# Kernel tuning notes

Measured on AMD Instinct MI355X. Metric: run time of the kernel, lower is better.

Reference implementation:

```python
import jax, jax.numpy as jnp
import numpy as np
from jax import lax

DN = ('NCHW', 'OIHW', 'NCHW')
EPS = 1e-5


def _conv3x3(x, w, b):
    return lax.conv_general_dilated(x, w, (1, 1), 'SAME', dimension_numbers=DN) + b[:, None, None]


def _conv1x1(x, w, b):
    return jnp.einsum('bchw,oc->bohw', x, w) + b[:, None, None]


def _dwconv3x3(x, w, b):
    # w: (C,1,3,3), depthwise
    C = x.shape[1]
    return lax.conv_general_dilated(x, w, (1, 1), 'SAME', feature_group_count=C,
                                    dimension_numbers=DN) + b[:, None, None]


def setup_inputs() -> dict:
    key = jax.random.key(0)
    ks = jax.random.split(key, 24)
    b, t, c, h, w = 2, 8, 64, 160, 160
    r, K = c // 4, 3

    def n(k, shape, s=0.05):
        return jax.random.normal(k, shape, dtype=jnp.float32) * s

    return {
        'feature': n(ks[0], (b, t, c, h, w), 1.0),
        'kc_w1': n(ks[1], (r, c)),
        'kc_bn_gamma': jnp.ones((r,), jnp.float32),
        'kc_bn_beta': jnp.zeros((r,), jnp.float32),
        'kc_bn_mean': jnp.zeros((r,), jnp.float32),
        'kc_bn_var': jnp.ones((r,), jnp.float32),
        'kc_w2': n(ks[2], (c * K * K, r)),
        'kc_b2': n(ks[3], (c * K * K,)),
        'kc_bias': n(ks[4], (c,)),
        'conv1_w': n(ks[5], (2 * c, 2 * c, 3, 3)),
        'conv1_b': n(ks[6], (2 * c,)),
        'pi1_w': n(ks[7], (4 * c, c)),
        'pi1_b': n(ks[8], (4 * c,)),
        'dw1_w': n(ks[9], (4 * c, 1, 3, 3)),
        'dw1_b': n(ks[10], (4 * c,)),
        'po1_w': n(ks[11], (c, 4 * c)),
        'po1_b': n(ks[12], (c,)),
        'pi2_w': n(ks[13], (4 * c, c)),
        'pi2_b': n(ks[14], (4 * c,)),
        'dw2_w': n(ks[15], (4 * c, 1, 3, 3)),
        'dw2_b': n(ks[16], (4 * c,)),
        'po2_w': n(ks[17], (c, 4 * c)),
        'po2_b': n(ks[18], (c,)),
    }


def reference(feature, kc_w1, kc_bn_gamma, kc_bn_beta, kc_bn_mean, kc_bn_var,
              kc_w2, kc_b2, kc_bias, conv1_w, conv1_b,
              pi1_w, pi1_b, dw1_w, dw1_b, po1_w, po1_b,
              pi2_w, pi2_b, dw2_w, dw2_b, po2_w, po2_b):
    b, t, c, h, w = feature.shape
    K = int(round((kc_w2.shape[0] // c) ** 0.5))  # dynamic kernel size (3)

    def dyn_dwconv(x_feat, y):
        # kernel generation: GAP -> 1x1 -> BN(eval) -> ReLU -> 1x1
        pool = x_feat.mean(axis=(2, 3))                           # (b, c)
        z = pool @ kc_w1.T                                        # (b, r)
        z = (z - kc_bn_mean) * jax.lax.rsqrt(kc_bn_var + EPS) * kc_bn_gamma + kc_bn_beta
        z = jax.nn.relu(z)
        wd = (z @ kc_w2.T + kc_b2).reshape(b, c, K, K)            # per-sample dw kernels

        def per_sample(yi, wi):
            return lax.conv_general_dilated(yi[None], wi[:, None], (1, 1), 'SAME',
                                            feature_group_count=c,
                                            dimension_numbers=DN)[0]
        out = jax.vmap(per_sample)(y, wd)                         # (b, c, h, w)
        return out + kc_bias[None, :, None, None]

    def step(feat_prop, x_feat):
        fp = dyn_dwconv(x_feat, feat_prop)
        fusion = jnp.concatenate([x_feat, fp], axis=1)
        fusion = jax.nn.leaky_relu(_conv3x3(fusion, conv1_w, conv1_b), 0.1)
        f1, f2 = fusion[:, :c], fusion[:, c:]
        g1 = jax.nn.sigmoid(_conv1x1(_dwconv3x3(_conv1x1(f1, pi1_w, pi1_b), dw1_w, dw1_b), po1_w, po1_b))
        g2 = jax.nn.sigmoid(_conv1x1(_dwconv3x3(_conv1x1(f2, pi2_w, pi2_b), dw2_w, dw2_b), po2_w, po2_b))
        new_fp = f1 * g1 + f2 * g2
        return new_fp, new_fp

    init = feature[:, t - 1]                                      # frame t-1
    xs = jnp.moveaxis(jnp.flip(feature[:, :t - 1], axis=1), 1, 0)  # frames t-2 .. 0
    _, ys = lax.scan(step, init, xs)                              # (t-1, b, c, h, w)
    full = jnp.concatenate([jnp.flip(ys, axis=0), init[None]], axis=0)
    return jnp.moveaxis(full, 0, 1)                               # (b, t, c, h, w)
```

## Files before the change

### kernel.cpp

```cpp
#include <hip/hip_runtime.h>

typedef __attribute__((ext_vector_type(8))) __bf16 bf16x8;
typedef __attribute__((ext_vector_type(4))) float f32x4;

#define BB 2
#define TT 8
#define CC 64
#define HH 160
#define WW 160
#define HWW 25600
#define RR 16
#define C2 128
#define C4 256
#define C8 512
#define NSTEP 7
#define CHW (CC*HWW)
#define EPSV 1e-5f

__device__ __forceinline__ f32x4 mfma16(bf16x8 a, bf16x8 b, f32x4 c) {
    return __builtin_amdgcn_mfma_f32_16x16x32_bf16(a, b, c, 0, 0, 0);
}

__global__ void pool_kernel(const float* __restrict__ feat, float* __restrict__ pool) {
    int idx = blockIdx.x;
    int b = idx / (NSTEP * CC);
    int f = (idx / CC) % NSTEP;
    int c = idx % CC;
    const float4* src = (const float4*)(feat + ((size_t)(b * TT + f) * CC + c) * HWW);
    float s = 0.f;
    for (int i = threadIdx.x; i < HWW / 4; i += 256) {
        float4 v = src[i];
        s += v.x + v.y + v.z + v.w;
    }
    __shared__ float sm[256];
    sm[threadIdx.x] = s;
    __syncthreads();
    for (int off = 128; off > 0; off >>= 1) {
        if (threadIdx.x < off) sm[threadIdx.x] += sm[threadIdx.x + off];
        __syncthreads();
    }
    if (threadIdx.x == 0) pool[idx] = sm[0] * (1.0f / HWW);
}

__global__ void wd_kernel(const float* __restrict__ pool, const float* __restrict__ w1,
                          const float* __restrict__ gamma, const float* __restrict__ beta,
                          const float* __restrict__ mean, const float* __restrict__ var,
                          const float* __restrict__ w2, const float* __restrict__ b2,
                          float* __restrict__ wdT) {
    int bf = blockIdx.x;
    __shared__ float z[RR];
    int tid = threadIdx.x;
    if (tid < RR) {
        const float* p = pool + bf * CC;
        float s = 0.f;
        for (int c = 0; c < CC; c++) s += p[c] * w1[tid * CC + c];
        s = (s - mean[tid]) * rsqrtf(var[tid] + EPSV) * gamma[tid] + beta[tid];
        z[tid] = s > 0.f ? s : 0.f;
    }
    __syncthreads();
    for (int o = tid; o < CC * 9; o += 64) {
        float s = b2[o];
        #pragma unroll
        for (int r = 0; r < RR; r++) s += z[r] * w2[o * RR + r];
        int c = o / 9, t = o % 9;
        wdT[bf * 576 + t * CC + c] = s;
    }
}

__global__ void copy_init_kernel(const float* __restrict__ feat, float* __restrict__ out) {
    int i = blockIdx.x * 256 + threadIdx.x;
    int n4 = CHW / 4;
    int b = i / n4;
    int r = i % n4;
    size_t off = ((size_t)(b * TT + (TT - 1)) * CHW) / 4 + r;
    ((float4*)out)[off] = ((const float4*)feat)[off];
}

__global__ void prep_weights(const float* __restrict__ c1w,
                             const float* __restrict__ pi1, const float* __restrict__ pi2,
                             const float* __restrict__ po1, const float* __restrict__ po2,
                             const float* __restrict__ dw1, const float* __restrict__ dw2,
                             const float* __restrict__ dw1b, const float* __restrict__ dw2b,
                             __bf16* __restrict__ Bc1,
                             __bf16* __restrict__ Bpi1, __bf16* __restrict__ Bpi2,
                             __bf16* __restrict__ Bpo1, __bf16* __restrict__ Bpo2,
                             float* __restrict__ dwT12, float* __restrict__ dwb12) {
    int idx = blockIdx.x * 256 + threadIdx.x;
    if (idx < 147456) {
        int oc = idx / 1152, k = idx % 1152;
        int t = k >> 7, ic = k & 127;
        Bc1[idx] = (__bf16)c1w[(oc * 128 + ic) * 9 + t];
        return;
    }
    idx -= 147456;
    if (idx < 16384) { Bpi1[idx] = (__bf16)pi1[idx]; return; }
    idx -= 16384;
    if (idx < 16384) { Bpi2[idx] = (__bf16)pi2[idx]; return; }
    idx -= 16384;
    if (idx < 16384) { Bpo1[idx] = (__bf16)po1[idx]; return; }
    idx -= 16384;
    if (idx < 16384) { Bpo2[idx] = (__bf16)po2[idx]; return; }
    idx -= 16384;
    if (idx < 4608) {
        int t = idx / 512, c = idx % 512;
        dwT12[t * C8 + c] = (c < 256) ? dw1[c * 9 + t] : dw2[(c - 256) * 9 + t];
        return;
    }
    idx -= 4608;
    if (idx < 512) { dwb12[idx] = (idx < 256) ? dw1b[idx] : dw2b[idx - 256]; }
}

__global__ void featPM_kernel(const float* __restrict__ feat, __bf16* __restrict__ featPM) {
    __shared__ float Lt[64 * 68];
    int bf = blockIdx.x / 400;
    int p0 = (blockIdx.x % 400) * 64;
    int tid = threadIdx.x;
    int c = tid & 63, half = tid >> 6;
    const float* src = feat + ((size_t)bf * CC + c) * HWW + p0 + half * 16;
    #pragma unroll
    for (int k = 0; k < 16; k++) Lt[(half * 16 + k) * 68 + c] = src[k];
    __syncthreads();
    int cg = tid & 7;
    #pragma unroll
    for (int pass = 0; pass < 2; pass++) {
        int pl = (tid >> 3) + pass * 32;
        bf16x8 o;
        #pragma unroll
        for (int j = 0; j < 8; j++) o[j] = (__bf16)Lt[pl * 68 + cg * 8 + j];
        *(bf16x8*)(featPM + ((size_t)bf * HWW + p0 + pl) * CC + cg * 8) = o;
    }
}

__global__ void dyndw_kernel(const __bf16* __restrict__ src, size_t bstr,
                             const float* __restrict__ wdT, const float* __restrict__ kc_bias,
                             __bf16* __restrict__ fpPM, int fx) {
    int gi = blockIdx.x * 256 + threadIdx.x;
    int c0 = (gi & 7) * 8;
    int rem = gi >> 3;
    int p = rem % HWW;
    int bb = rem / HWW;
    int py = p / WW, px = p % WW;
    float acc[8];
    float4 k0 = *(const float4*)(kc_bias + c0);
    float4 k1 = *(const float4*)(kc_bias + c0 + 4);
    acc[0]=k0.x; acc[1]=k0.y; acc[2]=k0.z; acc[3]=k0.w;
    acc[4]=k1.x; acc[5]=k1.y; acc[6]=k1.z; acc[7]=k1.w;
    const float* wb = wdT + (size_t)(bb * NSTEP + fx) * 576;
    const __bf16* sb = src + (size_t)bb * bstr;
    const int dyA[9] = {-1,-1,-1,0,0,0,1,1,1};
    const int dxA[9] = {-1,0,1,-1,0,1,-1,0,1};
    #pragma unroll
    for (int t = 0; t < 9; t++) {
        int dy = dyA[t], dx = dxA[t];
        if ((unsigned)(py + dy) < HH && (unsigned)(px + dx) < WW) {
            bf16x8 uv = *(const bf16x8*)(sb + (size_t)(p + dy * WW + dx) * CC + c0);
            float4 w0 = *(const float4*)(wb + t * CC + c0);
            float4 w1 = *(const float4*)(wb + t * CC + c0 + 4);
            acc[0] += (float)uv[0] * w0.x; acc[1] += (float)uv[1] * w0.y;
            acc[2] += (float)uv[2] * w0.z; acc[3] += (float)uv[3] * w0.w;
            acc[4] += (float)uv[4] * w1.x; acc[5] += (float)uv[5] * w1.y;
            acc[6] += (float)uv[6] * w1.z; acc[7] += (float)uv[7] * w1.w;
        }
    }
    bf16x8 o;
    #pragma unroll
    for (int j = 0; j < 8; j++) o[j] = (__bf16)acc[j];
    *(bf16x8*)(fpPM + ((size_t)bb * HWW + p) * CC + c0) = o;
}

__global__ void conv1_gemm(const __bf16* __restrict__ featPM, const __bf16* __restrict__ fpPM,
                           const __bf16* __restrict__ Bc1, const float* __restrict__ bias,
                           __bf16* __restrict__ fusionPM, int fx) {
    __shared__ __align__(16) __bf16 As[128 * 40];
    __shared__ __align__(16) __bf16 Bs[128 * 40];
    const int tid = threadIdx.x;
    const int bb = blockIdx.x / 200;
    const int p0 = (blockIdx.x % 200) * 128;
    const int i = tid >> 1, h = tid & 1;
    const int p = p0 + i;
    const int py = p / WW, px = p % WW;
    const __bf16* featB = featPM + (size_t)(bb * TT + fx) * HWW * CC;
    const __bf16* fpB   = fpPM + (size_t)bb * HWW * CC;
    const int wv = tid >> 6, lane = tid & 63, lm = lane & 15, lq = lane >> 4;
    f32x4 acc[2][8];
    #pragma unroll
    for (int mt = 0; mt < 2; mt++)
        #pragma unroll
        for (int nt = 0; nt < 8; nt++) acc[mt][nt] = (f32x4){0.f, 0.f, 0.f, 0.f};

    for (int ks = 0; ks < 36; ks++) {
        const int t = ks >> 2, ci0 = (ks & 3) * 32;
        const int dy = t / 3 - 1, dx = t % 3 - 1;
        const bool valid = ((unsigned)(py + dy) < HH) && ((unsigned)(px + dx) < WW);
        uint4 a0 = {0,0,0,0}, a1 = {0,0,0,0};
        if (valid) {
            const __bf16* sp = (ci0 < 64)
                ? featB + (size_t)(p + dy * WW + dx) * CC + ci0
                : fpB   + (size_t)(p + dy * WW + dx) * CC + (ci0 - 64);
            a0 = *(const uint4*)(sp + h * 16);
            a1 = *(const uint4*)(sp + h * 16 + 8);
        }
        const __bf16* bp = Bc1 + (size_t)i * 1152 + ks * 32 + h * 16;
        uint4 w0q = *(const uint4*)(bp);
        uint4 w1q = *(const uint4*)(bp + 8);
        __syncthreads();
        *(uint4*)&As[i * 40 + h * 16]     = a0;
        *(uint4*)&As[i * 40 + h * 16 + 8] = a1;
        *(uint4*)&Bs[i * 40 + h * 16]     = w0q;
        *(uint4*)&Bs[i * 40 + h * 16 + 8] = w1q;
        __syncthreads();
        bf16x8 af0 = *(const bf16x8*)&As[((wv * 2 + 0) * 16 + lm) * 40 + lq * 8];
        bf16x8 af1 = *(const bf16x8*)&As[((wv * 2 + 1) * 16 + lm) * 40 + lq * 8];
        #pragma unroll
        for (int nt = 0; nt < 8; nt++) {
            bf16x8 bf = *(const bf16x8*)&Bs[(nt * 16 + lm) * 40 + lq * 8];
            acc[0][nt] = mfma16(af0, bf, acc[0][nt]);
            acc[1][nt] = mfma16(af1, bf, acc[1][nt]);
        }
    }
    __bf16* ob = fusionPM + (size_t)bb * HWW * C2;
    #pragma unroll
    for (int mt = 0; mt < 2; mt++) {
        #pragma unroll
        for (int nt = 0; nt < 8; nt++) {
            const int oc = nt * 16 + lm;
            const float bs = bias[oc];
            #pragma unroll
            for (int r = 0; r < 4; r++) {
                const int pp = p0 + (wv * 2 + mt) * 16 + lq * 4 + r;
                float v = acc[mt][nt][r] + bs;
                v = v > 0.f ? v : 0.1f * v;
                ob[(size_t)pp * C2 + oc] = (__bf16)v;
            }
        }
    }
}

__global__ void pw1_gemm(const __bf16* __restrict__ fusionPM,
                         const __bf16* __restrict__ Bpi1, const __bf16* __restrict__ Bpi2,
                         const float* __restrict__ pi1b, const float* __restrict__ pi2b,
                         __bf16* __restrict__ u12PM) {
    __shared__ __align__(16) __bf16 As[128 * 40];
    __shared__ __align__(16) __bf16 Bs[128 * 40];
    const int tid = threadIdx.x;
    const int bb = blockIdx.x / 800;
    const int rem = blockIdx.x % 800;
    const int p0 = (rem >> 2) * 128;
    const int nb = rem & 3;
    const int br = nb >> 1, ns = nb & 1;
    const __bf16* Bpi = br ? Bpi2 : Bpi1;
    const float* bias = br ? pi2b : pi1b;
    const int i = tid >> 1, h = tid & 1;
    const int p = p0 + i;
    const __bf16* fB = fusionPM + (size_t)bb * HWW * C2 + br * CC;
    const int wv = tid >> 6, lane = tid & 63, lm = lane & 15, lq = lane >> 4;
    f32x4 acc[2][8];
    #pragma unroll
    for (int mt = 0; mt < 2; mt++)
        #pragma unroll
        for (int nt = 0; nt < 8; nt++) acc[mt][nt] = (f32x4){0.f, 0.f, 0.f, 0.f};

    #pragma unroll
    for (int ks = 0; ks < 2; ks++) {
        const int ci0 = ks * 32;
        const __bf16* sp = fB + (size_t)p * C2 + ci0 + h * 16;
        uint4 a0 = *(const uint4*)(sp);
        uint4 a1 = *(const uint4*)(sp + 8);
        const __bf16* bp = Bpi + (size_t)(ns * 128 + i) * 64 + ci0 + h * 16;
        uint4 w0q = *(const uint4*)(bp);
        uint4 w1q = *(const uint4*)(bp + 8);
        __syncthreads();
        *(uint4*)&As[i * 40 + h * 16]     = a0;
        *(uint4*)&As[i * 40 + h * 16 + 8] = a1;
        *(uint4*)&Bs[i * 40 + h * 16]     = w0q;
        *(uint4*)&Bs[i * 40 + h * 16 + 8] = w1q;
        __syncthreads();
        bf16x8 af0 = *(const bf16x8*)&As[((wv * 2 + 0) * 16 + lm) * 40 + lq * 8];
        bf16x8 af1 = *(const bf16x8*)&As[((wv * 2 + 1) * 16 + lm) * 40 + lq * 8];
        #pragma unroll
        for (int nt = 0; nt < 8; nt++) {
            bf16x8 bf = *(const bf16x8*)&Bs[(nt * 16 + lm) * 40 + lq * 8];
            acc[0][nt] = mfma16(af0, bf, acc[0][nt]);
            acc[1][nt] = mfma16(af1, bf, acc[1][nt]);
        }
    }
    __bf16* ub = u12PM + (size_t)bb * HWW * C8;
    #pragma unroll
    for (int mt = 0; mt < 2; mt++) {
        #pragma unroll
        for (int nt = 0; nt < 8; nt++) {
            const int ocl = ns * 128 + nt * 16 + lm;
            const int oc = br * 256 + ocl;
            const float bs = bias[ocl];
            #pragma unroll
            for (int r = 0; r < 4; r++) {
                const int pp = p0 + (wv * 2 + mt) * 16 + lq * 4 + r;
                ub[(size_t)pp * C8 + oc] = (__bf16)(acc[mt][nt][r] + bs);
            }
        }
    }
}

__global__ void dwv_kernel(const __bf16* __restrict__ u12PM, const float* __restrict__ dwT12,
                           const float* __restrict__ dwb12, __bf16* __restrict__ v12PM) {
    int gi = blockIdx.x * 256 + threadIdx.x;
    int c0 = (gi & 63) * 8;
    int rem = gi >> 6;
    int p = rem % HWW;
    int bb = rem / HWW;
    int py = p / WW, px = p % WW;
    float acc[8];
    float4 b0 = *(const float4*)(dwb12 + c0);
    float4 b1 = *(const float4*)(dwb12 + c0 + 4);
    acc[0]=b0.x; acc[1]=b0.y; acc[2]=b0.z; acc[3]=b0.w;
    acc[4]=b1.x; acc[5]=b1.y; acc[6]=b1.z; acc[7]=b1.w;
    const __bf16* ub = u12PM + (size_t)bb * HWW * C8;
    const int dyA[9] = {-1,-1,-1,0,0,0,1,1,1};
    const int dxA[9] = {-1,0,1,-1,0,1,-1,0,1};
    #pragma unroll
    for (int t = 0; t < 9; t++) {
        int dy = dyA[t], dx = dxA[t];
        if ((unsigned)(py + dy) < HH && (unsigned)(px + dx) < WW) {
            bf16x8 uv = *(const bf16x8*)(ub + (size_t)(p + dy * WW + dx) * C8 + c0);
            float4 w0 = *(const float4*)(dwT12 + t * C8 + c0);
            float4 w1 = *(const float4*)(dwT12 + t * C8 + c0 + 4);
            acc[0] += (float)uv[0] * w0.x; acc[1] += (float)uv[1] * w0.y;
            acc[2] += (float)uv[2] * w0.z; acc[3] += (float)uv[3] * w0.w;
            acc[4] += (float)uv[4] * w1.x; acc[5] += (float)uv[5] * w1.y;
            acc[6] += (float)uv[6] * w1.z; acc[7] += (float)uv[7] * w1.w;
        }
    }
    bf16x8 o;
    #pragma unroll
    for (int j = 0; j < 8; j++) o[j] = (__bf16)acc[j];
    *(bf16x8*)(v12PM + ((size_t)bb * HWW + p) * C8 + c0) = o;
}

__global__ void pw2_gemm(const __bf16* __restrict__ v12PM,
                         const __bf16* __restrict__ Bpo1, const __bf16* __restrict__ Bpo2,
                         const float* __restrict__ pob1, const float* __restrict__ pob2,
                         const __bf16* __restrict__ fusionPM,
                         float* __restrict__ out, __bf16* __restrict__ outPM, int fx) {
    __shared__ __align__(16) __bf16 As[128 * 40];
    __shared__ __align__(16) __bf16 Bs[64 * 40];
    const int tid = threadIdx.x;
    const int bb = blockIdx.x / 200;
    const int p0 = (blockIdx.x % 200) * 128;
    const int i = tid >> 1, h = tid & 1;
    const int p = p0 + i;
    const __bf16* vB = v12PM + (size_t)bb * HWW * C8;
    const int wv = tid >> 6, lane = tid & 63, lm = lane & 15, lq = lane >> 4;
    f32x4 acc[2][2][4];
    #pragma unroll
    for (int br = 0; br < 2; br++)
        #pragma unroll
        for (int mt = 0; mt < 2; mt++)
            #pragma unroll
            for (int nt = 0; nt < 4; nt++) acc[br][mt][nt] = (f32x4){0.f, 0.f, 0.f, 0.f};

    for (int ks = 0; ks < 16; ks++) {
        const int ci0 = ks * 32;
        const int br = ks >> 3;
        const __bf16* sp = vB + (size_t)p * C8 + ci0 + h * 16;
        uint4 a0 = *(const uint4*)(sp);
        uint4 a1 = *(const uint4*)(sp + 8);
        uint4 w0q = {0,0,0,0}, w1q = {0,0,0,0};
        if (tid < 128) {
            const __bf16* Bpo = br ? Bpo2 : Bpo1;
            const __bf16* bp = Bpo + (size_t)i * C4 + (ci0 & 255) + h * 16;
            w0q = *(const uint4*)(bp);
            w1q = *(const uint4*)(bp + 8);
        }
        __syncthreads();
        *(uint4*)&As[i * 40 + h * 16]     = a0;
        *(uint4*)&As[i * 40 + h * 16 + 8] = a1;
        if (tid < 128) {
            *(uint4*)&Bs[i * 40 + h * 16]     = w0q;
            *(uint4*)&Bs[i * 40 + h * 16 + 8] = w1q;
        }
        __syncthreads();
        bf16x8 af0 = *(const bf16x8*)&As[((wv * 2 + 0) * 16 + lm) * 40 + lq * 8];
        bf16x8 af1 = *(const bf16x8*)&As[((wv * 2 + 1) * 16 + lm) * 40 + lq * 8];
        #pragma unroll
        for (int nt = 0; nt < 4; nt++) {
            bf16x8 bf = *(const bf16x8*)&Bs[(nt * 16 + lm) * 40 + lq * 8];
            acc[br][0][nt] = mfma16(af0, bf, acc[br][0][nt]);
            acc[br][1][nt] = mfma16(af1, bf, acc[br][1][nt]);
        }
    }
    const __bf16* fB = fusionPM + (size_t)bb * HWW * C2;
    __bf16* opB = outPM + (size_t)bb * HWW * CC;
    #pragma unroll
    for (int mt = 0; mt < 2; mt++) {
        #pragma unroll
        for (int nt = 0; nt < 4; nt++) {
            const int oc = nt * 16 + lm;
            const float bs1 = pob1[oc];
            const float bs2 = pob2[oc];
            #pragma unroll
            for (int r = 0; r < 4; r++) {
                const int pp = p0 + (wv * 2 + mt) * 16 + lq * 4 + r;
                float g1 = 1.f / (1.f + __expf(-(acc[0][mt][nt][r] + bs1)));
                float g2 = 1.f / (1.f + __expf(-(acc[1][mt][nt][r] + bs2)));
                float f1 = (float)fB[(size_t)pp * C2 + oc];
                float f2 = (float)fB[(size_t)pp * C2 + CC + oc];
                float val = f1 * g1 + f2 * g2;
                out[((size_t)(bb * TT + fx) * CC + oc) * HWW + pp] = val;
                opB[(size_t)pp * CC + oc] = (__bf16)val;
            }
        }
    }
}

extern "C" void kernel_launch(void* const* d_in, const int* in_sizes, int n_in,
                              void* d_out, int out_size, void* d_ws, size_t ws_size,
                              hipStream_t stream) {
    const float* feat     = (const float*)d_in[0];
    const float* kc_w1    = (const float*)d_in[1];
    const float* kc_g     = (const float*)d_in[2];
    const float* kc_be    = (const float*)d_in[3];
    const float* kc_mu    = (const float*)d_in[4];
    const float* kc_var   = (const float*)d_in[5];
    const float* kc_w2    = (const float*)d_in[6];
    const float* kc_b2    = (const float*)d_in[7];
    const float* kc_bias  = (const float*)d_in[8];
    const float* conv1_w  = (const float*)d_in[9];
    const float* conv1_b  = (const float*)d_in[10];
    const float* pi1_w    = (const float*)d_in[11];
    const float* pi1_b    = (const float*)d_in[12];
    const float* dw1_w    = (const float*)d_in[13];
    const float* dw1_b    = (const float*)d_in[14];
    const float* po1_w    = (const float*)d_in[15];
    const float* po1_b    = (const float*)d_in[16];
    const float* pi2_w    = (const float*)d_in[17];
    const float* pi2_b    = (const float*)d_in[18];
    const float* dw2_w    = (const float*)d_in[19];
    const float* dw2_b    = (const float*)d_in[20];
    const float* po2_w    = (const float*)d_in[21];
    const float* po2_b    = (const float*)d_in[22];
    float* out = (float*)d_out;

    char* W = (char*)d_ws;
    __bf16* featPM   = (__bf16*)W; W += (size_t)BB * TT * HWW * CC * 2;
    __bf16* fpPM     = (__bf16*)W; W += (size_t)BB * HWW * CC * 2;
    __bf16* fusionPM = (__bf16*)W; W += (size_t)BB * HWW * C2 * 2;
    __bf16* u12PM    = (__bf16*)W; W += (size_t)BB * HWW * C8 * 2;
    __bf16* v12PM    = (__bf16*)W; W += (size_t)BB * HWW * C8 * 2;
    __bf16* outPM    = (__bf16*)W; W += (size_t)BB * HWW * CC * 2;
    __bf16* Bc1      = (__bf16*)W; W += 294912;
    __bf16* Bpi1     = (__bf16*)W; W += 32768;
    __bf16* Bpi2     = (__bf16*)W; W += 32768;
    __bf16* Bpo1     = (__bf16*)W; W += 32768;
    __bf16* Bpo2     = (__bf16*)W; W += 32768;
    float*  dwT12    = (float*)W;  W += 18432;
    float*  dwb12    = (float*)W;  W += 2048;
    float*  poolb    = (float*)W;  W += 4096;
    float*  wdT      = (float*)W;  W += 32256;

    prep_weights<<<852, 256, 0, stream>>>(conv1_w, pi1_w, pi2_w, po1_w, po2_w, dw1_w, dw2_w,
                                          dw1_b, dw2_b,
                                          Bc1, Bpi1, Bpi2, Bpo1, Bpo2, dwT12, dwb12);
    featPM_kernel<<<BB * TT * 400, 256, 0, stream>>>(feat, featPM);
    pool_kernel<<<BB * NSTEP * CC, 256, 0, stream>>>(feat, poolb);
    wd_kernel<<<BB * NSTEP, 64, 0, stream>>>(poolb, kc_w1, kc_g, kc_be, kc_mu, kc_var, kc_w2, kc_b2, wdT);
    copy_init_kernel<<<BB * CHW / 4 / 256, 256, 0, stream>>>(feat, out);

    for (int i = 0; i < NSTEP; i++) {
        int fx = NSTEP - 1 - i;
        const __bf16* src = (fx == NSTEP - 1) ? (featPM + (size_t)(TT - 1) * HWW * CC) : outPM;
        size_t bstr = (fx == NSTEP - 1) ? (size_t)TT * HWW * CC : (size_t)HWW * CC;
        dyndw_kernel<<<BB * HWW * 8 / 256, 256, 0, stream>>>(src, bstr, wdT, kc_bias, fpPM, fx);
        conv1_gemm<<<BB * 200, 256, 0, stream>>>(featPM, fpPM, Bc1, conv1_b, fusionPM, fx);
        pw1_gemm<<<BB * 800, 256, 0, stream>>>(fusionPM, Bpi1, Bpi2, pi1_b, pi2_b, u12PM);
        dwv_kernel<<<BB * HWW * 64 / 256, 256, 0, stream>>>(u12PM, dwT12, dwb12, v12PM);
        pw2_gemm<<<BB * 200, 256, 0, stream>>>(v12PM, Bpo1, Bpo2, po1_b, po2_b, fusionPM, out, outPM, fx);
    }
}
```

Before: 1.147 ms.

## Fuse pointwise-in, depthwise and pointwise-out gate stages into one tiled kernel

Replaces the three kernels pw1_gemm, dwv_kernel and pw2_gemm with a single gate_fused kernel. Each 512-thread block handles a 16x16 spatial tile. It recomputes the expanded 512-channel activations for an 18x18 halo tile in LDS in 32-channel chunks, applies the depthwise 3x3 from LDS, and accumulates the output projection in registers. This removes the large u12/v12 intermediate buffers and their global-memory round trips, which were the dominant traffic. In exchange it redoes halo work and uses only 200 blocks at one block per CU, so occupancy is low and barriers are serialized per chunk.

```diff
diff --git a/kernel.cpp b/kernel.cpp
--- a/kernel.cpp
+++ b/kernel.cpp
@@ -16,6 +16,8 @@
 #define NSTEP 7
 #define CHW (CC*HWW)
 #define EPSV 1e-5f
+#define UPITCH 40
+#define VPITCH 40
 
 __device__ __forceinline__ f32x4 mfma16(bf16x8 a, bf16x8 b, f32x4 c) {
     return __builtin_amdgcn_mfma_f32_16x16x32_bf16(a, b, c, 0, 0, 0);
@@ -236,177 +238,145 @@
     }
 }
 
-__global__ void pw1_gemm(const __bf16* __restrict__ fusionPM,
-                         const __bf16* __restrict__ Bpi1, const __bf16* __restrict__ Bpi2,
-                         const float* __restrict__ pi1b, const float* __restrict__ pi2b,
-                         __bf16* __restrict__ u12PM) {
-    __shared__ __align__(16) __bf16 As[128 * 40];
-    __shared__ __align__(16) __bf16 Bs[128 * 40];
+__global__ __launch_bounds__(512, 1)
+void gate_fused(const __bf16* __restrict__ fusionPM,
+                const __bf16* __restrict__ Bpi1, const __bf16* __restrict__ Bpi2,
+                const float* __restrict__ pi1b, const float* __restrict__ pi2b,
+                const __bf16* __restrict__ Bpo1, const __bf16* __restrict__ Bpo2,
+                const float* __restrict__ pob1, const float* __restrict__ pob2,
+                const float* __restrict__ dwT12, const float* __restrict__ dwb12,
+                float* __restrict__ out, __bf16* __restrict__ outPM, int fx) {
+    __shared__ __align__(16) __bf16 Us[336 * UPITCH];
+    __shared__ __align__(16) __bf16 Vs[256 * VPITCH];
     const int tid = threadIdx.x;
-    const int bb = blockIdx.x / 800;
-    const int rem = blockIdx.x % 800;
-    const int p0 = (rem >> 2) * 128;
-    const int nb = rem & 3;
-    const int br = nb >> 1, ns = nb & 1;
-    const __bf16* Bpi = br ? Bpi2 : Bpi1;
-    const float* bias = br ? pi2b : pi1b;
-    const int i = tid >> 1, h = tid & 1;
-    const int p = p0 + i;
-    const __bf16* fB = fusionPM + (size_t)bb * HWW * C2 + br * CC;
+    const int bb = blockIdx.x / 100;
+    const int tile = blockIdx.x % 100;
+    const int py0 = (tile / 10) * 16, px0 = (tile % 10) * 16;
     const int wv = tid >> 6, lane = tid & 63, lm = lane & 15, lq = lane >> 4;
-    f32x4 acc[2][8];
-    #pragma unroll
-    for (int mt = 0; mt < 2; mt++)
-        #pragma unroll
-        for (int nt = 0; nt < 8; nt++) acc[mt][nt] = (f32x4){0.f, 0.f, 0.f, 0.f};
-
-    #pragma unroll
-    for (int ks = 0; ks < 2; ks++) {
-        const int ci0 = ks * 32;
-        const __bf16* sp = fB + (size_t)p * C2 + ci0 + h * 16;
-        uint4 a0 = *(const uint4*)(sp);
-        uint4 a1 = *(const uint4*)(sp + 8);
-        const __bf16* bp = Bpi + (size_t)(ns * 128 + i) * 64 + ci0 + h * 16;
-        uint4 w0q = *(const uint4*)(bp);
-        uint4 w1q = *(const uint4*)(bp + 8);
+    const __bf16* fB = fusionPM + (size_t)bb * HWW * C2;
+
+    f32x4 acc2[2][2][4];
+    #pragma unroll
+    for (int b2 = 0; b2 < 2; b2++)
+        #pragma unroll
+        for (int m2 = 0; m2 < 2; m2++)
+            #pragma unroll
+            for (int nt = 0; nt < 4; nt++) acc2[b2][m2][nt] = (f32x4){0.f, 0.f, 0.f, 0.f};
+
+    auto ugemm = [&](int c) {
+        const int br = c >> 3, s = c & 7;
+        const __bf16* Bpi = br ? Bpi2 : Bpi1;
+        const float* pib = br ? pi2b : pi1b;
+        bf16x8 bfr[2][2];
+        #pragma unroll
+        for (int nt = 0; nt < 2; nt++)
+            #pragma unroll
+            for (int ks = 0; ks < 2; ks++)
+                bfr[nt][ks] = *(const bf16x8*)(Bpi + (size_t)(s * 32 + nt * 16 + lm) * 64 + ks * 32 + lq * 8);
+        for (int mt = wv; mt < 21; mt += 8) {
+            int j = mt * 16 + lm; if (j > 323) j = 323;
+            int hy = j / 18, hx = j % 18;
+            int gy = py0 - 1 + hy, gx = px0 - 1 + hx;
+            gy = gy < 0 ? 0 : (gy > 159 ? 159 : gy);
+            gx = gx < 0 ? 0 : (gx > 159 ? 159 : gx);
+            const __bf16* ap = fB + (size_t)(gy * WW + gx) * C2 + br * 64 + lq * 8;
+            bf16x8 a0 = *(const bf16x8*)ap;
+            bf16x8 a1 = *(const bf16x8*)(ap + 32);
+            #pragma unroll
+            for (int nt = 0; nt < 2; nt++) {
+                f32x4 uac = (f32x4){0.f, 0.f, 0.f, 0.f};
+                uac = mfma16(a0, bfr[nt][0], uac);
+                uac = mfma16(a1, bfr[nt][1], uac);
+                const float bs = pib[s * 32 + nt * 16 + lm];
+                #pragma unroll
+                for (int r = 0; r < 4; r++)
+                    Us[(mt * 16 + lq * 4 + r) * UPITCH + nt * 16 + lm] = (__bf16)(uac[r] + bs);
+            }
+        }
+    };
+
+    auto dwph = [&](int c) {
+        const int cb = (c >> 3) * 256 + (c & 7) * 32;
+        #pragma unroll
+        for (int k = 0; k < 2; k++) {
+            int idx = k * 512 + tid;
+            int pxl = idx & 255, grp = idx >> 8;
+            int ly = pxl >> 4, lx = pxl & 15;
+            int c0 = grp * 8;
+            float a[8];
+            float4 b0 = *(const float4*)(dwb12 + cb + c0);
+            float4 b1 = *(const float4*)(dwb12 + cb + c0 + 4);
+            a[0]=b0.x; a[1]=b0.y; a[2]=b0.z; a[3]=b0.w;
+            a[4]=b1.x; a[5]=b1.y; a[6]=b1.z; a[7]=b1.w;
+            #pragma unroll
+            for (int t = 0; t < 9; t++) {
+                int dy = t / 3 - 1, dx = t % 3 - 1;
+                int gy = py0 + ly + dy, gx = px0 + lx + dx;
+                if ((unsigned)gy < HH && (unsigned)gx < WW) {
+                    int h = (ly + 1 + dy) * 18 + (lx + 1 + dx);
+                    bf16x8 uv = *(const bf16x8*)&Us[h * UPITCH + c0];
+                    float4 w0 = *(const float4*)(dwT12 + t * C8 + cb + c0);
+                    float4 w1 = *(const float4*)(dwT12 + t * C8 + cb + c0 + 4);
+                    a[0] += (float)uv[0] * w0.x; a[1] += (float)uv[1] * w0.y;
+                    a[2] += (float)uv[2] * w0.z; a[3] += (float)uv[3] * w0.w;
+                    a[4] += (float)uv[4] * w1.x; a[5] += (float)uv[5] * w1.y;
+                    a[6] += (float)uv[6] * w1.z; a[7] += (float)uv[7] * w1.w;
+                }
+            }
+            bf16x8 o;
+            #pragma unroll
+            for (int j = 0; j < 8; j++) o[j] = (__bf16)a[j];
+            *(bf16x8*)&Vs[pxl * VPITCH + c0] = o;
+        }
+    };
+
+    auto vgemm = [&](int c) {
+        const int br = c >> 3, s = c & 7;
+        const __bf16* Bpo = br ? Bpo2 : Bpo1;
+        bf16x8 bv[4];
+        #pragma unroll
+        for (int nt = 0; nt < 4; nt++)
+            bv[nt] = *(const bf16x8*)(Bpo + (size_t)(nt * 16 + lm) * C4 + s * 32 + lq * 8);
+        #pragma unroll
+        for (int m2 = 0; m2 < 2; m2++) {
+            int mt = wv * 2 + m2;
+            bf16x8 av = *(const bf16x8*)&Vs[(mt * 16 + lm) * VPITCH + lq * 8];
+            #pragma unroll
+            for (int nt = 0; nt < 4; nt++)
+                acc2[br][m2][nt] = mfma16(av, bv[nt], acc2[br][m2][nt]);
+        }
+    };
+
+    ugemm(0);
+    __syncthreads();
+    for (int c = 0; c < 16; c++) {
+        dwph(c);
         __syncthreads();
-        *(uint4*)&As[i * 40 + h * 16]     = a0;
-        *(uint4*)&As[i * 40 + h * 16 + 8] = a1;
-        *(uint4*)&Bs[i * 40 + h * 16]     = w0q;
-        *(uint4*)&Bs[i * 40 + h * 16 + 8] = w1q;
+        vgemm(c);
+        if (c < 15) ugemm(c + 1);
         __syncthreads();
-        bf16x8 af0 = *(const bf16x8*)&As[((wv * 2 + 0) * 16 + lm) * 40 + lq * 8];
-        bf16x8 af1 = *(const bf16x8*)&As[((wv * 2 + 1) * 16 + lm) * 40 + lq * 8];
-        #pragma unroll
-        for (int nt = 0; nt < 8; nt++) {
-            bf16x8 bf = *(const bf16x8*)&Bs[(nt * 16 + lm) * 40 + lq * 8];
-            acc[0][nt] = mfma16(af0, bf, acc[0][nt]);
-            acc[1][nt] = mfma16(af1, bf, acc[1][nt]);
-        }
-    }
-    __bf16* ub = u12PM + (size_t)bb * HWW * C8;
-    #pragma unroll
-    for (int mt = 0; mt < 2; mt++) {
-        #pragma unroll
-        for (int nt = 0; nt < 8; nt++) {
-            const int ocl = ns * 128 + nt * 16 + lm;
-            const int oc = br * 256 + ocl;
-            const float bs = bias[ocl];
-            #pragma unroll
-            for (int r = 0; r < 4; r++) {
-                const int pp = p0 + (wv * 2 + mt) * 16 + lq * 4 + r;
-                ub[(size_t)pp * C8 + oc] = (__bf16)(acc[mt][nt][r] + bs);
-            }
-        }
-    }
-}
-
-__global__ void dwv_kernel(const __bf16* __restrict__ u12PM, const float* __restrict__ dwT12,
-                           const float* __restrict__ dwb12, __bf16* __restrict__ v12PM) {
-    int gi = blockIdx.x * 256 + threadIdx.x;
-    int c0 = (gi & 63) * 8;
-    int rem = gi >> 6;
-    int p = rem % HWW;
-    int bb = rem / HWW;
-    int py = p / WW, px = p % WW;
-    float acc[8];
-    float4 b0 = *(const float4*)(dwb12 + c0);
-    float4 b1 = *(const float4*)(dwb12 + c0 + 4);
-    acc[0]=b0.x; acc[1]=b0.y; acc[2]=b0.z; acc[3]=b0.w;
-    acc[4]=b1.x; acc[5]=b1.y; acc[6]=b1.z; acc[7]=b1.w;
-    const __bf16* ub = u12PM + (size_t)bb * HWW * C8;
-    const int dyA[9] = {-1,-1,-1,0,0,0,1,1,1};
-    const int dxA[9] = {-1,0,1,-1,0,1,-1,0,1};
-    #pragma unroll
-    for (int t = 0; t < 9; t++) {
-        int dy = dyA[t], dx = dxA[t];
-        if ((unsigned)(py + dy) < HH && (unsigned)(px + dx) < WW) {
-            bf16x8 uv = *(const bf16x8*)(ub + (size_t)(p + dy * WW + dx) * C8 + c0);
-            float4 w0 = *(const float4*)(dwT12 + t * C8 + c0);
-            float4 w1 = *(const float4*)(dwT12 + t * C8 + c0 + 4);
-            acc[0] += (float)uv[0] * w0.x; acc[1] += (float)uv[1] * w0.y;
-            acc[2] += (float)uv[2] * w0.z; acc[3] += (float)uv[3] * w0.w;
-            acc[4] += (float)uv[4] * w1.x; acc[5] += (float)uv[5] * w1.y;
-            acc[6] += (float)uv[6] * w1.z; acc[7] += (float)uv[7] * w1.w;
-        }
-    }
-    bf16x8 o;
-    #pragma unroll
-    for (int j = 0; j < 8; j++) o[j] = (__bf16)acc[j];
-    *(bf16x8*)(v12PM + ((size_t)bb * HWW + p) * C8 + c0) = o;
-}
-
-__global__ void pw2_gemm(const __bf16* __restrict__ v12PM,
-                         const __bf16* __restrict__ Bpo1, const __bf16* __restrict__ Bpo2,
-                         const float* __restrict__ pob1, const float* __restrict__ pob2,
-                         const __bf16* __restrict__ fusionPM,
-                         float* __restrict__ out, __bf16* __restrict__ outPM, int fx) {
-    __shared__ __align__(16) __bf16 As[128 * 40];
-    __shared__ __align__(16) __bf16 Bs[64 * 40];
-    const int tid = threadIdx.x;
-    const int bb = blockIdx.x / 200;
-    const int p0 = (blockIdx.x % 200) * 128;
-    const int i = tid >> 1, h = tid & 1;
-    const int p = p0 + i;
-    const __bf16* vB = v12PM + (size_t)bb * HWW * C8;
-    const int wv = tid >> 6, lane = tid & 63, lm = lane & 15, lq = lane >> 4;
-    f32x4 acc[2][2][4];
-    #pragma unroll
-    for (int br = 0; br < 2; br++)
-        #pragma unroll
-        for (int mt = 0; mt < 2; mt++)
-            #pragma unroll
-            for (int nt = 0; nt < 4; nt++) acc[br][mt][nt] = (f32x4){0.f, 0.f, 0.f, 0.f};
-
-    for (int ks = 0; ks < 16; ks++) {
-        const int ci0 = ks * 32;
-        const int br = ks >> 3;
-        const __bf16* sp = vB + (size_t)p * C8 + ci0 + h * 16;
-        uint4 a0 = *(const uint4*)(sp);
-        uint4 a1 = *(const uint4*)(sp + 8);
-        uint4 w0q = {0,0,0,0}, w1q = {0,0,0,0};
-        if (tid < 128) {
-            const __bf16* Bpo = br ? Bpo2 : Bpo1;
-            const __bf16* bp = Bpo + (size_t)i * C4 + (ci0 & 255) + h * 16;
-            w0q = *(const uint4*)(bp);
-            w1q = *(const uint4*)(bp + 8);
-        }
-        __syncthreads();
-        *(uint4*)&As[i * 40 + h * 16]     = a0;
-        *(uint4*)&As[i * 40 + h * 16 + 8] = a1;
-        if (tid < 128) {
-            *(uint4*)&Bs[i * 40 + h * 16]     = w0q;
-            *(uint4*)&Bs[i * 40 + h * 16 + 8] = w1q;
-        }
-        __syncthreads();
-        bf16x8 af0 = *(const bf16x8*)&As[((wv * 2 + 0) * 16 + lm) * 40 + lq * 8];
-        bf16x8 af1 = *(const bf16x8*)&As[((wv * 2 + 1) * 16 + lm) * 40 + lq * 8];
-        #pragma unroll
-        for (int nt = 0; nt < 4; nt++) {
-            bf16x8 bf = *(const bf16x8*)&Bs[(nt * 16 + lm) * 40 + lq * 8];
-            acc[br][0][nt] = mfma16(af0, bf, acc[br][0][nt]);
-            acc[br][1][nt] = mfma16(af1, bf, acc[br][1][nt]);
-        }
-    }
-    const __bf16* fB = fusionPM + (size_t)bb * HWW * C2;
+    }
+
     __bf16* opB = outPM + (size_t)bb * HWW * CC;
-    #pragma unroll
-    for (int mt = 0; mt < 2; mt++) {
+    float* oB = out + (size_t)(bb * TT + fx) * CHW;
+    #pragma unroll
+    for (int m2 = 0; m2 < 2; m2++) {
         #pragma unroll
         for (int nt = 0; nt < 4; nt++) {
             const int oc = nt * 16 + lm;
-            const float bs1 = pob1[oc];
-            const float bs2 = pob2[oc];
+            const float b1 = pob1[oc], b2 = pob2[oc];
             #pragma unroll
             for (int r = 0; r < 4; r++) {
-                const int pp = p0 + (wv * 2 + mt) * 16 + lq * 4 + r;
-                float g1 = 1.f / (1.f + __expf(-(acc[0][mt][nt][r] + bs1)));
-                float g2 = 1.f / (1.f + __expf(-(acc[1][mt][nt][r] + bs2)));
-                float f1 = (float)fB[(size_t)pp * C2 + oc];
-                float f2 = (float)fB[(size_t)pp * C2 + CC + oc];
+                int pxl = (wv * 2 + m2) * 16 + lq * 4 + r;
+                int gy = py0 + (pxl >> 4), gx = px0 + (pxl & 15);
+                int gp = gy * WW + gx;
+                float g1 = 1.f / (1.f + __expf(-(acc2[0][m2][nt][r] + b1)));
+                float g2 = 1.f / (1.f + __expf(-(acc2[1][m2][nt][r] + b2)));
+                float f1 = (float)fB[(size_t)gp * C2 + oc];
+                float f2 = (float)fB[(size_t)gp * C2 + CC + oc];
                 float val = f1 * g1 + f2 * g2;
-                out[((size_t)(bb * TT + fx) * CC + oc) * HWW + pp] = val;
-                opB[(size_t)pp * CC + oc] = (__bf16)val;
+                oB[(size_t)oc * HWW + gp] = val;
+                opB[(size_t)gp * CC + oc] = (__bf16)val;
             }
         }
     }
@@ -444,8 +414,6 @@
     __bf16* featPM   = (__bf16*)W; W += (size_t)BB * TT * HWW * CC * 2;
     __bf16* fpPM     = (__bf16*)W; W += (size_t)BB * HWW * CC * 2;
     __bf16* fusionPM = (__bf16*)W; W += (size_t)BB * HWW * C2 * 2;
-    __bf16* u12PM    = (__bf16*)W; W += (size_t)BB * HWW * C8 * 2;
-    __bf16* v12PM    = (__bf16*)W; W += (size_t)BB * HWW * C8 * 2;
     __bf16* outPM    = (__bf16*)W; W += (size_t)BB * HWW * CC * 2;
     __bf16* Bc1      = (__bf16*)W; W += 294912;
     __bf16* Bpi1     = (__bf16*)W; W += 32768;
@@ -471,8 +439,8 @@
         size_t bstr = (fx == NSTEP - 1) ? (size_t)TT * HWW * CC : (size_t)HWW * CC;
         dyndw_kernel<<<BB * HWW * 8 / 256, 256, 0, stream>>>(src, bstr, wdT, kc_bias, fpPM, fx);
         conv1_gemm<<<BB * 200, 256, 0, stream>>>(featPM, fpPM, Bc1, conv1_b, fusionPM, fx);
-        pw1_gemm<<<BB * 800, 256, 0, stream>>>(fusionPM, Bpi1, Bpi2, pi1_b, pi2_b, u12PM);
-        dwv_kernel<<<BB * HWW * 64 / 256, 256, 0, stream>>>(u12PM, dwT12, dwb12, v12PM);
-        pw2_gemm<<<BB * 200, 256, 0, stream>>>(v12PM, Bpo1, Bpo2, po1_b, po2_b, fusionPM, out, outPM, fx);
-    }
-}
+        gate_fused<<<BB * 100, 512, 0, stream>>>(fusionPM, Bpi1, Bpi2, pi1_b, pi2_b,
+                                                 Bpo1, Bpo2, po1_b, po2_b,
+                                                 dwT12, dwb12, out, outPM, fx);
+    }
+}
```

After: 1.757 ms. 1.53x slower.
